# Performance work log

Hardware: AMD Instinct MI355X
Metric: run time of the kernel (lower is better)

Reference implementation:

```python
import jax, jax.numpy as jnp
import numpy as np
from jax import lax


def setup_inputs() -> dict:
    key = jax.random.key(0)
    ks = jax.random.split(key, 6)
    B, C, H, W = 8, 128, 64, 64   # C = 2*channel, channel (per-branch) c = 64
    c = C // 2
    return {
        "x_up": jax.random.normal(ks[0], (B, C, H, W), dtype=jnp.float32),
        "x_skip": jax.random.normal(ks[1], (B, C, H, W), dtype=jnp.float32),
        # nn.Linear(c, 2c): weight [out,in], bias [out]
        "kv1_w": jax.random.normal(ks[2], (2 * c, c), dtype=jnp.float32) * 0.05,
        "kv1_b": jnp.zeros((2 * c,), dtype=jnp.float32),
        "kv2_w": jax.random.normal(ks[3], (2 * c, c), dtype=jnp.float32) * 0.05,
        "kv2_b": jnp.zeros((2 * c,), dtype=jnp.float32),
        # Conv2d(2c, 2c, 3, stride 1, pad 1, bias=False), OIHW
        "conv_w": jax.random.normal(ks[4], (C, C, 3, 3), dtype=jnp.float32) * 0.05,
        # BatchNorm2d(2c) in inference form (running stats)
        "bn_gamma": jax.random.normal(ks[5], (C,), dtype=jnp.float32) * 0.1 + 1.0,
        "bn_beta": jnp.zeros((C,), dtype=jnp.float32),
        "bn_mean": jnp.zeros((C,), dtype=jnp.float32),
        "bn_var": jnp.ones((C,), dtype=jnp.float32),
    }


def reference(x_up, x_skip, kv1_w, kv1_b, kv2_w, kv2_b, conv_w,
              bn_gamma, bn_beta, bn_mean, bn_var):
    b, C, h, w = x_up.shape
    c = C // 2
    hw = h * w
    up1, up2 = x_up[:, :c], x_up[:, c:]
    sk1, sk2 = x_skip[:, :c], x_skip[:, c:]

    # ---- spatial attention branch (softmax over last axis, hw x hw) ----
    shortcut1 = up1 + sk1
    u1 = up1.reshape(b, c, hw).transpose(0, 2, 1)   # (b, hw, c)
    s1 = sk1.reshape(b, c, hw).transpose(0, 2, 1)   # (b, hw, c)
    kv = s1 @ kv1_w.T + kv1_b                        # (b, hw, 2c)
    k1, v1 = kv[..., :c], kv[..., c:]
    attn = jax.nn.softmax(jnp.einsum('bnc,bmc->bnm', u1, k1), axis=-1)  # (b, hw, hw)
    sout = jnp.einsum('bnm,bmc->bnc', attn, v1)      # (b, hw, c)
    sout = sout.transpose(0, 2, 1).reshape(b, c, h, w) + shortcut1

    # ---- channel attention branch (softmax over dim=1 of the c x c map) ----
    shortcut2 = up2 + sk2
    u2 = up2.reshape(b, c, hw).transpose(0, 2, 1)    # (b, hw, c)
    s2 = sk2.reshape(b, c, hw).transpose(0, 2, 1)
    kv = s2 @ kv2_w.T + kv2_b                        # (b, hw, 2c)
    k2, v2 = kv[..., :c], kv[..., c:]
    A = jax.nn.softmax(jnp.einsum('bnc,bnd->bcd', u2, k2), axis=1)  # (b, c, c)
    cout = jnp.einsum('bnc,bcd->bnd', v2, A)          # (b, hw, c)
    cout = cout.transpose(0, 2, 1).reshape(b, c, h, w) + shortcut2

    # ---- conv + BN (inference) + ReLU ----
    x = jnp.concatenate([sout, cout], axis=1)         # (b, 2c, h, w)
    y = lax.conv_general_dilated(x, conv_w, (1, 1), 'SAME',
                                 dimension_numbers=('NCHW', 'OIHW', 'NCHW'))
    inv = jax.lax.rsqrt(bn_var + 1e-5)
    y = (y - bn_mean[None, :, None, None]) * (inv * bn_gamma)[None, :, None, None] \
        + bn_beta[None, :, None, None]
    return jax.nn.relu(y)
```

## Files before the change

### kernel.cpp

```cpp
#include <hip/hip_runtime.h>
#include <math.h>

#define HW 4096

typedef __attribute__((ext_vector_type(8))) short bh8;
typedef __attribute__((ext_vector_type(4))) float f32x4;
typedef __attribute__((ext_vector_type(2))) unsigned int u32x2;
typedef unsigned int u32;
typedef unsigned short u16;

__device__ __forceinline__ u16 f2bf(float f) {
  union { float f; u32 u; } v; v.f = f;
  u32 u = v.u;
  return (u16)((u + 0x7FFFu + ((u >> 16) & 1u)) >> 16);
}
__device__ __forceinline__ float bf2f(u16 h) {
  union { u32 u; float f; } v; v.u = ((u32)h) << 16;
  return v.f;
}
__device__ __forceinline__ float ubits2f(u32 u) {
  union { u32 u; float f; } v; v.u = u;
  return v.f;
}
__device__ __forceinline__ u32 cvt_pk_bf16(float lo, float hi) {
  u32 r;
  asm("v_cvt_pk_bf16_f32 %0, %1, %2" : "=v"(r) : "v"(lo), "v"(hi));
  return r;
}
__device__ __forceinline__ float fexp2(float x) {
  float r;
  asm("v_exp_f32 %0, %1" : "=v"(r) : "v"(x));
  return r;
}

__global__ __launch_bounds__(256) void kv_proj(
    const float* __restrict__ xs,
    const float* __restrict__ w1, const float* __restrict__ b1,
    const float* __restrict__ w2, const float* __restrict__ b2,
    u32* __restrict__ Knm, u16* __restrict__ Vcm,
    u16* __restrict__ K2t, u16* __restrict__ V2t,
    const float* __restrict__ cw, const float* __restrict__ gamma,
    const float* __restrict__ beta, const float* __restrict__ mean,
    const float* __restrict__ var, u16* __restrict__ Wg,
    float* __restrict__ shb, float* __restrict__ M) {
  __shared__ __align__(16) u16 XsH[64][72];
  __shared__ __align__(16) u16 XsL[64][72];
  __shared__ u32 LtK[64][33];
  const int b = blockIdx.y, n0 = blockIdx.x * 64;
  const int t = threadIdx.x;
  const int wq = t >> 6, lane = t & 63, lq = lane & 15, quad = lane >> 4;
  const float* xsb = xs + (size_t)b * 128 * HW;

  {
    int gid = (blockIdx.y * 64 + blockIdx.x) * 256 + t;
    for (int i = gid; i < 147456; i += 131072) {
      int tap = i >> 14, oc = (i >> 7) & 127, ic = i & 127;
      float sc = gamma[oc] * rsqrtf(var[oc] + 1e-5f);
      Wg[i] = f2bf(cw[((size_t)(oc * 128 + ic)) * 9 + tap] * sc);
    }
    if (gid < 128) {
      float sc = gamma[gid] * rsqrtf(var[gid] + 1e-5f);
      shb[gid] = beta[gid] - mean[gid] * sc;
    }
    if (gid < 32768) M[gid] = 0.f;
  }

  for (int br = 0; br < 2; ++br) {
    const float* W = br ? w2 : w1;
    const float* bias = br ? b2 : b1;
    const float* src = xsb + (br ? 64 * HW : 0);

    bh8 wh[2][2], wl[2][2];
#pragma unroll
    for (int jt = 0; jt < 2; ++jt)
#pragma unroll
      for (int s = 0; s < 2; ++s) {
        const float* wr = W + (size_t)(wq * 32 + jt * 16 + lq) * 64 + s * 32 + quad * 8;
        float4 a0 = *(const float4*)wr;
        float4 a1 = *(const float4*)(wr + 4);
        float f[8] = {a0.x, a0.y, a0.z, a0.w, a1.x, a1.y, a1.z, a1.w};
        union { u32 u[4]; bh8 v; } H, L;
#pragma unroll
        for (int p = 0; p < 4; ++p) {
          u32 hp = cvt_pk_bf16(f[2 * p], f[2 * p + 1]);
          float h0 = ubits2f(hp << 16);
          float h1 = ubits2f(hp & 0xFFFF0000u);
          H.u[p] = hp;
          L.u[p] = cvt_pk_bf16(f[2 * p] - h0, f[2 * p + 1] - h1);
        }
        wh[jt][s] = H.v;
        wl[jt][s] = L.v;
      }

    if (br) __syncthreads();
    {
      const int n = t & 63, cg = t >> 6;
#pragma unroll
      for (int s8 = 0; s8 < 8; ++s8) {
        int ch0 = s8 * 8 + cg * 2;
        float f0 = src[(size_t)ch0 * HW + n0 + n];
        float f1 = src[(size_t)(ch0 + 1) * HW + n0 + n];
        u32 hp = cvt_pk_bf16(f0, f1);
        float h0 = ubits2f(hp << 16);
        float h1 = ubits2f(hp & 0xFFFF0000u);
        u32 lp = cvt_pk_bf16(f0 - h0, f1 - h1);
        *(u32*)&XsH[n][ch0] = hp;
        *(u32*)&XsL[n][ch0] = lp;
      }
    }
    __syncthreads();

    f32x4 acc[2][4];
#pragma unroll
    for (int nt = 0; nt < 4; ++nt) {
      const int xr = nt * 16 + lq;
      bh8 xh0 = *(const bh8*)&XsH[xr][quad * 8];
      bh8 xh1 = *(const bh8*)&XsH[xr][32 + quad * 8];
      bh8 xl0 = *(const bh8*)&XsL[xr][quad * 8];
      bh8 xl1 = *(const bh8*)&XsL[xr][32 + quad * 8];
#pragma unroll
      for (int jt = 0; jt < 2; ++jt) {
        f32x4 a = (f32x4)(0.f);
        a = __builtin_amdgcn_mfma_f32_16x16x32_bf16(wh[jt][0], xh0, a, 0, 0, 0);
        a = __builtin_amdgcn_mfma_f32_16x16x32_bf16(wh[jt][1], xh1, a, 0, 0, 0);
        a = __builtin_amdgcn_mfma_f32_16x16x32_bf16(wh[jt][0], xl0, a, 0, 0, 0);
        a = __builtin_amdgcn_mfma_f32_16x16x32_bf16(wh[jt][1], xl1, a, 0, 0, 0);
        a = __builtin_amdgcn_mfma_f32_16x16x32_bf16(wl[jt][0], xh0, a, 0, 0, 0);
        a = __builtin_amdgcn_mfma_f32_16x16x32_bf16(wl[jt][1], xh1, a, 0, 0, 0);
        acc[jt][nt] = a;
      }
    }

    if (br == 0) {
      if (wq < 2) {
#pragma unroll
        for (int jt = 0; jt < 2; ++jt) {
          float4 bv = *(const float4*)&bias[wq * 32 + jt * 16 + quad * 4];
#pragma unroll
          for (int nt = 0; nt < 4; ++nt) {
            f32x4 a = acc[jt][nt];
            LtK[nt * 16 + lq][wq * 16 + jt * 8 + quad * 2] =
                cvt_pk_bf16(a[0] + bv.x, a[1] + bv.y);
            LtK[nt * 16 + lq][wq * 16 + jt * 8 + quad * 2 + 1] =
                cvt_pk_bf16(a[2] + bv.z, a[3] + bv.w);
          }
        }
      } else {
#pragma unroll
        for (int jt = 0; jt < 2; ++jt) {
          float4 bv = *(const float4*)&bias[wq * 32 + jt * 16 + quad * 4];
          float bvv[4] = {bv.x, bv.y, bv.z, bv.w};
#pragma unroll
          for (int nt = 0; nt < 4; ++nt)
#pragma unroll
            for (int r = 0; r < 4; ++r) {
              int ch = (wq - 2) * 32 + jt * 16 + quad * 4 + r;
              Vcm[((size_t)b * 64 + ch) * HW + n0 + nt * 16 + lq] =
                  f2bf(acc[jt][nt][r] + bvv[r]);
            }
        }
      }
      __syncthreads();
#pragma unroll
      for (int p = 0; p < 8; ++p) {
        int idx = p * 256 + t;
        int n = idx >> 5, cc = idx & 31;
        Knm[((size_t)b * HW + n0 + n) * 32 + cc] = LtK[n][cc];
      }
    } else {
      u16* base = (wq < 2) ? (K2t + (size_t)b * 64 * HW) : (V2t + (size_t)b * 64 * HW);
      const int chb = (wq & 1) * 32;
#pragma unroll
      for (int jt = 0; jt < 2; ++jt) {
        float4 bv = *(const float4*)&bias[wq * 32 + jt * 16 + quad * 4];
        float bvv[4] = {bv.x, bv.y, bv.z, bv.w};
#pragma unroll
        for (int nt = 0; nt < 4; ++nt)
#pragma unroll
          for (int r = 0; r < 4; ++r) {
            int ch = chb + jt * 16 + quad * 4 + r;
            base[(size_t)ch * HW + n0 + nt * 16 + lq] =
                f2bf(acc[jt][nt][r] + bvv[r]);
          }
      }
    }
  }
}

__device__ __forceinline__ void qk_step(
    const bh8* kf, const bh8 (&qb)[4][2], f32x4 (&S)[2][4]) {
  __builtin_amdgcn_s_setprio(1);
#pragma unroll
  for (int mt = 0; mt < 2; ++mt)
#pragma unroll
    for (int nt = 0; nt < 4; ++nt) {
      f32x4 a = (f32x4)(0.f);
      a = __builtin_amdgcn_mfma_f32_16x16x32_bf16(kf[mt * 2 + 0], qb[nt][0], a, 0, 0, 0);
      a = __builtin_amdgcn_mfma_f32_16x16x32_bf16(kf[mt * 2 + 1], qb[nt][1], a, 0, 0, 0);
      S[mt][nt] = a;
    }
  __builtin_amdgcn_s_setprio(0);
}

__device__ __forceinline__ void sm_pv(
    const f32x4 (&S)[2][4], const bh8* vf, const bh8 ones,
    f32x4 (&O)[4][4], f32x4 (&Osum)[4]) {
#pragma unroll
  for (int nt = 0; nt < 4; ++nt) {
    const float c = 17.312340f;
    float e00 = fexp2(S[0][nt][0] - c), e01 = fexp2(S[0][nt][1] - c);
    float e02 = fexp2(S[0][nt][2] - c), e03 = fexp2(S[0][nt][3] - c);
    float e10 = fexp2(S[1][nt][0] - c), e11 = fexp2(S[1][nt][1] - c);
    float e12 = fexp2(S[1][nt][2] - c), e13 = fexp2(S[1][nt][3] - c);
    u32 A = cvt_pk_bf16(e00, e01);
    u32 B = cvt_pk_bf16(e02, e03);
    u32 C = cvt_pk_bf16(e10, e11);
    u32 D = cvt_pk_bf16(e12, e13);
    u32x2 rac = __builtin_amdgcn_permlane32_swap(A, C, 0, 0);
    u32x2 rbd = __builtin_amdgcn_permlane32_swap(B, D, 0, 0);
    u32x2 r02 = __builtin_amdgcn_permlane16_swap(rac.x, rac.y, 0, 0);
    u32x2 r13 = __builtin_amdgcn_permlane16_swap(rbd.x, rbd.y, 0, 0);
    union { u32 u[4]; bh8 v; } pb;
    pb.u[0] = r02.x;
    pb.u[1] = r13.x;
    pb.u[2] = r02.y;
    pb.u[3] = r13.y;
    __builtin_amdgcn_s_setprio(1);
#pragma unroll
    for (int ct = 0; ct < 4; ++ct)
      O[ct][nt] = __builtin_amdgcn_mfma_f32_16x16x32_bf16(vf[ct], pb.v, O[ct][nt], 0, 0, 0);
    Osum[nt] = __builtin_amdgcn_mfma_f32_16x16x32_bf16(ones, pb.v, Osum[nt], 0, 0, 0);
    __builtin_amdgcn_s_setprio(0);
  }
}

#define LOADKV(KB, KF, VF)                                            \
  do {                                                                \
    const int n0_ = (KB) * 128;                                       \
    const u16* kr_ = Kb + (size_t)(n0_ + wb + lq) * 64 + quad * 8;    \
    KF[0] = *(const bh8*)(kr_);                                       \
    KF[1] = *(const bh8*)(kr_ + 32);                                  \
    KF[2] = *(const bh8*)(kr_ + 1024);                                \
    KF[3] = *(const bh8*)(kr_ + 1056);                                \
    const u16* vr_ = Vb + (size_t)lq * HW + n0_ + wb + quad * 8;      \
    VF[0] = *(const bh8*)(vr_);                                       \
    VF[1] = *(const bh8*)(vr_ + 16 * HW);                             \
    VF[2] = *(const bh8*)(vr_ + 32 * HW);                             \
    VF[3] = *(const bh8*)(vr_ + 48 * HW);                             \
  } while (0)

__global__ __launch_bounds__(256, 2) void attn_gram(
    const float* __restrict__ xu, const float* __restrict__ xs,
    const u16* __restrict__ Knm, const u16* __restrict__ Vcm,
    u16* __restrict__ xcat,
    const u16* __restrict__ K2t, float* __restrict__ M) {
  __shared__ __align__(16) u16 SMEM[18432];
  const int b = blockIdx.y;
  const int t = threadIdx.x;
  const int wq = t >> 6, lane = t & 63, lq = lane & 15, quad = lane >> 4;

  if (blockIdx.x >= 64) {
    const int chunk = blockIdx.x - 64;
    const int nn = chunk * 128;
    const float* ub = xu + ((size_t)b * 128 + 64) * HW;
    const u16* kb2 = K2t + (size_t)b * 64 * HW;
    f32x4 acc[4];
#pragma unroll
    for (int ct = 0; ct < 4; ++ct) acc[ct] = (f32x4)(0.f);
#pragma unroll
    for (int kc = 0; kc < 4; ++kc) {
      const int nb2 = nn + kc * 32 + quad * 8;
      bh8 kb_ = *(const bh8*)&kb2[(size_t)(wq * 16 + lq) * HW + nb2];
#pragma unroll
      for (int ct = 0; ct < 4; ++ct) {
        const float* ar = ub + (size_t)(ct * 16 + lq) * HW + nb2;
        float4 a0 = *(const float4*)ar;
        float4 a1 = *(const float4*)(ar + 4);
        float f[8] = {a0.x, a0.y, a0.z, a0.w, a1.x, a1.y, a1.z, a1.w};
        union { u32 u[4]; bh8 v; } H, L;
#pragma unroll
        for (int p = 0; p < 4; ++p) {
          u32 hp = cvt_pk_bf16(f[2 * p], f[2 * p + 1]);
          float h0 = ubits2f(hp << 16);
          float h1 = ubits2f(hp & 0xFFFF0000u);
          H.u[p] = hp;
          L.u[p] = cvt_pk_bf16(f[2 * p] - h0, f[2 * p + 1] - h1);
        }
        acc[ct] = __builtin_amdgcn_mfma_f32_16x16x32_bf16(H.v, kb_, acc[ct], 0, 0, 0);
        acc[ct] = __builtin_amdgcn_mfma_f32_16x16x32_bf16(L.v, kb_, acc[ct], 0, 0, 0);
      }
    }
    float* Mb = M + (size_t)b * 4096;
#pragma unroll
    for (int ct = 0; ct < 4; ++ct)
#pragma unroll
      for (int r = 0; r < 4; ++r)
        atomicAdd(&Mb[(ct * 16 + quad * 4 + r) * 64 + wq * 16 + lq], acc[ct][r]);
    return;
  }

  const int q0 = blockIdx.x * 64;
  const int wb = wq * 32;
  const float* xub = xu + (size_t)b * 128 * HW;
  const float* xsb = xs + (size_t)b * 128 * HW;
  const u16* Kb = Knm + (size_t)b * HW * 64;
  const u16* Vb = Vcm + (size_t)b * 64 * HW;

  bh8 qb[4][2];
#pragma unroll
  for (int nt = 0; nt < 4; ++nt)
#pragma unroll
    for (int s = 0; s < 2; ++s)
#pragma unroll
      for (int j = 0; j < 8; ++j) {
        int ch = s * 32 + quad * 8 + j;
        qb[nt][s][j] =
            (short)f2bf(xub[(size_t)ch * HW + q0 + nt * 16 + lq] * 1.44269504f);
      }
  bh8 ones;
#pragma unroll
  for (int j = 0; j < 8; ++j) ones[j] = (short)0x3F80;

  f32x4 O[4][4];
#pragma unroll
  for (int ct = 0; ct < 4; ++ct)
#pragma unroll
    for (int nt = 0; nt < 4; ++nt) O[ct][nt] = (f32x4)(0.f);
  f32x4 Osum[4];
#pragma unroll
  for (int nt = 0; nt < 4; ++nt) Osum[nt] = (f32x4)(0.f);

  bh8 kfa[4], vfa[4], kfb[4], vfb[4];
  f32x4 Sa[2][4], Sb[2][4];
  LOADKV(0, kfa, vfa);
  qk_step(kfa, qb, Sa);
  LOADKV(1, kfb, vfb);
  for (int kb = 0; kb < 32; kb += 2) {
    qk_step(kfb, qb, Sb);
    sm_pv(Sa, vfa, ones, O, Osum);
    if (kb + 2 < 32) {
      LOADKV(kb + 2, kfa, vfa);
      qk_step(kfa, qb, Sa);
    }
    sm_pv(Sb, vfb, ones, O, Osum);
    if (kb + 3 < 32) LOADKV(kb + 3, kfb, vfb);
  }

  float* Posc = (float*)SMEM;
  float* Lred = (float*)(SMEM + 17408);
  if (quad == 0) {
#pragma unroll
    for (int nt = 0; nt < 4; ++nt) Lred[(wq * 4 + nt) * 16 + lq] = Osum[nt][0];
  }

  const int q = t & 63, cg = t >> 6;
#pragma unroll
  for (int rh = 0; rh < 2; ++rh) {
    if (rh) __syncthreads();
#pragma unroll
    for (int c2 = 0; c2 < 2; ++c2)
#pragma unroll
      for (int nt = 0; nt < 4; ++nt)
#pragma unroll
        for (int r = 0; r < 4; ++r)
          Posc[(wq * 32 + c2 * 16 + quad * 4 + r) * 68 + nt * 16 + lq] =
              O[rh * 2 + c2][nt][r];
    __syncthreads();
    float li = 0.f;
#pragma unroll
    for (int w2 = 0; w2 < 4; ++w2) li += Lred[w2 * 64 + q];
    float inv = 1.f / li;
    u16 h[8];
#pragma unroll
    for (int i = 0; i < 8; ++i) {
      int chl = cg * 8 + i;
      float s = 0.f;
#pragma unroll
      for (int w2 = 0; w2 < 4; ++w2) s += Posc[(w2 * 32 + chl) * 68 + q];
      int ch = rh * 32 + chl;
      size_t g = (size_t)ch * HW + q0 + q;
      h[i] = f2bf(s * inv + xub[g] + xsb[g]);
    }
    u32 pk[4];
#pragma unroll
    for (int j = 0; j < 4; ++j) pk[j] = (u32)h[2 * j] | ((u32)h[2 * j + 1] << 16);
    u16* ob = xcat + ((size_t)b * HW + q0 + q) * 128 + rh * 32 + cg * 8;
    *(uint4*)ob = make_uint4(pk[0], pk[1], pk[2], pk[3]);
  }
}

__global__ __launch_bounds__(256) void chan_apply(
    const u16* __restrict__ V2t, const float* __restrict__ M,
    const float* __restrict__ xu, const float* __restrict__ xs,
    u16* __restrict__ xcat) {
  __shared__ float Vsm[64][65];
  __shared__ float As[64][65];
  __shared__ float red1[4][64], red2[4][64];
  const int b = blockIdx.y, n0 = blockIdx.x * 64, t = threadIdx.x;
  const int lane = t & 63, dg = t >> 6;
  const u16* Vb = V2t + (size_t)b * 64 * HW;
  for (int s = 0; s < 16; ++s) {
    int c = s * 4 + dg;
    Vsm[lane][c] = bf2f(Vb[(size_t)c * HW + n0 + lane]);
  }
  for (int idx = t; idx < 4096; idx += 256) As[idx >> 6][idx & 63] = M[b * 4096 + idx];
  __syncthreads();
  float mx = -1e30f;
#pragma unroll
  for (int i = 0; i < 16; ++i) mx = fmaxf(mx, As[dg * 16 + i][lane]);
  red1[dg][lane] = mx;
  __syncthreads();
  mx = fmaxf(fmaxf(red1[0][lane], red1[1][lane]), fmaxf(red1[2][lane], red1[3][lane]));
  float se = 0.f;
#pragma unroll
  for (int i = 0; i < 16; ++i) {
    float e = __expf(As[dg * 16 + i][lane] - mx);
    As[dg * 16 + i][lane] = e;
    se += e;
  }
  red2[dg][lane] = se;
  __syncthreads();

  float acc[16];
#pragma unroll
  for (int i = 0; i < 16; ++i) acc[i] = 0.f;
  for (int c = 0; c < 64; ++c) {
    float v = Vsm[lane][c];
#pragma unroll
    for (int i = 0; i < 16; ++i) acc[i] = fmaf(v, As[c][dg * 16 + i], acc[i]);
  }
  const float* xub = xu + ((size_t)b * 128 + 64) * HW;
  const float* xsb = xs + ((size_t)b * 128 + 64) * HW;
  const int n = n0 + lane;
  u16 hv[16];
#pragma unroll
  for (int i = 0; i < 16; ++i) {
    int d = dg * 16 + i;
    float sm = red2[0][d] + red2[1][d] + red2[2][d] + red2[3][d];
    hv[i] = f2bf(acc[i] / sm + xub[(size_t)d * HW + n] + xsb[(size_t)d * HW + n]);
  }
  u32 pk[8];
#pragma unroll
  for (int j = 0; j < 8; ++j) pk[j] = (u32)hv[2 * j] | ((u32)hv[2 * j + 1] << 16);
  u16* ob = xcat + ((size_t)b * HW + n) * 128 + 64 + dg * 16;
  *(uint4*)(ob) = make_uint4(pk[0], pk[1], pk[2], pk[3]);
  *(uint4*)(ob + 8) = make_uint4(pk[4], pk[5], pk[6], pk[7]);
}

__global__ __launch_bounds__(512) void conv_mfma(
    const u16* __restrict__ X, const u16* __restrict__ Wg,
    const float* __restrict__ shb, float* __restrict__ out) {
  __shared__ __align__(16) u16 In[4 * 66 * 136];
  __shared__ __align__(16) u16 Wt[2][128 * 136];
  const int b = blockIdx.y, h0 = blockIdx.x * 2;
  const int t = threadIdx.x;
  const int wq = t >> 6, lane = t & 63, lq = lane & 15, quad = lane >> 4;
  const int nb = (wq & 1) * 64;
  const int mb = (wq >> 1) * 2;
  const u16* Xb = X + (size_t)b * HW * 128;

  if (t < 128) {
    int ih = t >> 5, iwsel = (t >> 4) & 1, ck = t & 15;
    int iw = iwsel ? 65 : 0;
    *(uint4*)&In[(ih * 66 + iw) * 136 + ck * 8] = make_uint4(0, 0, 0, 0);
  }
  for (int ih = 0; ih < 4; ++ih) {
    int h = h0 - 1 + ih;
    bool ok = (h >= 0 && h < 64);
    const u16* src = Xb + (size_t)h * 64 * 128;
#pragma unroll
    for (int p = 0; p < 2; ++p) {
      int idx = p * 512 + t;
      int row = idx >> 4, ck = idx & 15;
      uint4 d = make_uint4(0, 0, 0, 0);
      if (ok) d = *(const uint4*)(src + (size_t)row * 128 + ck * 8);
      *(uint4*)&In[(ih * 66 + 1 + row) * 136 + ck * 8] = d;
    }
  }
  {
    const u16* src = Wg;
#pragma unroll
    for (int p = 0; p < 4; ++p) {
      int idx = p * 512 + t;
      int oc = idx >> 4, ck = idx & 15;
      uint4 d = *(const uint4*)(src + oc * 128 + ck * 8);
      *(uint4*)&Wt[0][oc * 136 + ck * 8] = d;
    }
  }
  __syncthreads();

  f32x4 acc[2][4];
#pragma unroll
  for (int mt = 0; mt < 2; ++mt)
#pragma unroll
    for (int nt = 0; nt < 4; ++nt) acc[mt][nt] = (f32x4)(0.f);

  for (int tap = 0; tap < 9; ++tap) {
    const int cur = tap & 1;
    if (tap < 8) {
      const u16* src = Wg + (size_t)(tap + 1) * 128 * 128;
#pragma unroll
      for (int p = 0; p < 4; ++p) {
        int idx = p * 512 + t;
        int oc = idx >> 4, ck = idx & 15;
        uint4 d = *(const uint4*)(src + oc * 128 + ck * 8);
        *(uint4*)&Wt[cur ^ 1][oc * 136 + ck * 8] = d;
      }
    }
    const int dh = tap / 3, dw = tap - 3 * dh;
    const u16* Wc = &Wt[cur][0];
#pragma unroll
    for (int c = 0; c < 4; ++c) {
      bh8 bf[4];
#pragma unroll
      for (int nt = 0; nt < 4; ++nt)
        bf[nt] = *(const bh8*)&Wc[(nb + nt * 16 + lq) * 136 + c * 32 + quad * 8];
#pragma unroll
      for (int mt = 0; mt < 2; ++mt) {
        int s = (mb + mt) * 16 + lq;
        int ih = (s >> 6) + dh, iw = (s & 63) + dw;
        bh8 af = *(const bh8*)&In[(ih * 66 + iw) * 136 + c * 32 + quad * 8];
#pragma unroll
        for (int nt = 0; nt < 4; ++nt)
          acc[mt][nt] = __builtin_amdgcn_mfma_f32_16x16x32_bf16(af, bf[nt], acc[mt][nt], 0, 0, 0);
      }
    }
    __syncthreads();
  }

  float shv[4];
#pragma unroll
  for (int nt = 0; nt < 4; ++nt) shv[nt] = shb[nb + nt * 16 + lq];
#pragma unroll
  for (int mt = 0; mt < 2; ++mt) {
    int mtile = mb + mt;
    int h = h0 + (mtile >> 2);
    int w0 = ((mtile & 3) * 16) + quad * 4;
#pragma unroll
    for (int nt = 0; nt < 4; ++nt) {
      int oc = nb + nt * 16 + lq;
      float4 v;
      v.x = fmaxf(acc[mt][nt][0] + shv[nt], 0.f);
      v.y = fmaxf(acc[mt][nt][1] + shv[nt], 0.f);
      v.z = fmaxf(acc[mt][nt][2] + shv[nt], 0.f);
      v.w = fmaxf(acc[mt][nt][3] + shv[nt], 0.f);
      *(float4*)&out[((size_t)b * 128 + oc) * HW + h * 64 + w0] = v;
    }
  }
}

extern "C" void kernel_launch(void* const* d_in, const int* in_sizes, int n_in,
                              void* d_out, int out_size, void* d_ws, size_t ws_size,
                              hipStream_t stream) {
  const float* x_up   = (const float*)d_in[0];
  const float* x_skip = (const float*)d_in[1];
  const float* kv1_w  = (const float*)d_in[2];
  const float* kv1_b  = (const float*)d_in[3];
  const float* kv2_w  = (const float*)d_in[4];
  const float* kv2_b  = (const float*)d_in[5];
  const float* conv_w = (const float*)d_in[6];
  const float* bn_g   = (const float*)d_in[7];
  const float* bn_b   = (const float*)d_in[8];
  const float* bn_m   = (const float*)d_in[9];
  const float* bn_v   = (const float*)d_in[10];
  float* out = (float*)d_out;

  char* ws = (char*)d_ws;
  const size_t XCATB_B = (size_t)8 * HW * 128 * 2;
  const size_t KV16_B  = (size_t)8 * 64 * HW * 2;
  size_t off = 0;
  u16*   xcat = (u16*)(ws + off);   off += XCATB_B;
  u16*   K2t  = (u16*)(ws + off);   off += KV16_B;
  u16*   V2t  = (u16*)(ws + off);   off += KV16_B;
  u32*   Knm  = (u32*)(ws + off);   off += KV16_B;
  u16*   Vcm  = (u16*)(ws + off);   off += KV16_B;
  float* M    = (float*)(ws + off); off += (size_t)8 * 4096 * 4;
  u16*   Wg   = (u16*)(ws + off);   off += (size_t)9 * 128 * 128 * 2;
  float* shb  = (float*)(ws + off); off += 512;

  kv_proj<<<dim3(64, 8), 256, 0, stream>>>(x_skip, kv1_w, kv1_b, kv2_w, kv2_b,
                                           Knm, Vcm, K2t, V2t,
                                           conv_w, bn_g, bn_b, bn_m, bn_v, Wg,
                                           shb, M);
  attn_gram<<<dim3(96, 8), 256, 0, stream>>>(x_up, x_skip, (const u16*)Knm, Vcm,
                                             xcat, K2t, M);
  chan_apply<<<dim3(64, 8), 256, 0, stream>>>(V2t, M, x_up, x_skip, xcat);
  conv_mfma<<<dim3(32, 8), 512, 0, stream>>>(xcat, Wg, shb, out);
}
```

Measured before the change: 215.8 us.

## Flatten grids with batch-interleaved block ids and simplify attention pipeline

All four kernels now launch on a 1-D grid and derive the batch index from the low bits of the block id, so neighbouring blocks belong to different batches. On a multi-XCD GPU this spreads each batch's blocks across chiplets differently and changes L2 locality. The attention main loop also drops the software pipeline that overlapped QK of one tile with softmax/PV of the previous one. It replaces it with a fused per-tile step plus K/V prefetch, which lowers register pressure but gives up some MFMA/exp overlap.

Measured after the change: 207.1 us (median of 2 runs). 4.0% less time.

```diff
diff --git a/kernel.cpp b/kernel.cpp
--- a/kernel.cpp
+++ b/kernel.cpp
@@ -46,13 +46,14 @@
   __shared__ __align__(16) u16 XsH[64][72];
   __shared__ __align__(16) u16 XsL[64][72];
   __shared__ u32 LtK[64][33];
-  const int b = blockIdx.y, n0 = blockIdx.x * 64;
+  const int bid = blockIdx.x;
+  const int b = bid & 7, n0 = (bid >> 3) * 64;
   const int t = threadIdx.x;
   const int wq = t >> 6, lane = t & 63, lq = lane & 15, quad = lane >> 4;
   const float* xsb = xs + (size_t)b * 128 * HW;
 
   {
-    int gid = (blockIdx.y * 64 + blockIdx.x) * 256 + t;
+    int gid = bid * 256 + t;
     for (int i = gid; i < 147456; i += 131072) {
       int tap = i >> 14, oc = (i >> 7) & 127, ic = i & 127;
       float sc = gamma[oc] * rsqrtf(var[oc] + 1e-5f);
@@ -187,8 +188,10 @@
   }
 }
 
-__device__ __forceinline__ void qk_step(
-    const bh8* kf, const bh8 (&qb)[4][2], f32x4 (&S)[2][4]) {
+__device__ __forceinline__ void attn_step(
+    const bh8* kf, const bh8* vf, const bh8 (&qb)[4][2], const bh8 ones,
+    f32x4 (&O)[4][4], f32x4 (&Osum)[4]) {
+  f32x4 S[2][4];
   __builtin_amdgcn_s_setprio(1);
 #pragma unroll
   for (int mt = 0; mt < 2; ++mt)
@@ -200,11 +203,6 @@
       S[mt][nt] = a;
     }
   __builtin_amdgcn_s_setprio(0);
-}
-
-__device__ __forceinline__ void sm_pv(
-    const f32x4 (&S)[2][4], const bh8* vf, const bh8 ones,
-    f32x4 (&O)[4][4], f32x4 (&Osum)[4]) {
 #pragma unroll
   for (int nt = 0; nt < 4; ++nt) {
     const float c = 17.312340f;
@@ -255,12 +253,14 @@
     u16* __restrict__ xcat,
     const u16* __restrict__ K2t, float* __restrict__ M) {
   __shared__ __align__(16) u16 SMEM[18432];
-  const int b = blockIdx.y;
+  const int bid = blockIdx.x;
+  const int b = bid & 7;
+  const int x = bid >> 3;
   const int t = threadIdx.x;
   const int wq = t >> 6, lane = t & 63, lq = lane & 15, quad = lane >> 4;
 
-  if (blockIdx.x >= 64) {
-    const int chunk = blockIdx.x - 64;
+  if (x >= 64) {
+    const int chunk = x - 64;
     const int nn = chunk * 128;
     const float* ub = xu + ((size_t)b * 128 + 64) * HW;
     const u16* kb2 = K2t + (size_t)b * 64 * HW;
@@ -299,7 +299,7 @@
     return;
   }
 
-  const int q0 = blockIdx.x * 64;
+  const int q0 = x * 64;
   const int wb = wq * 32;
   const float* xub = xu + (size_t)b * 128 * HW;
   const float* xsb = xs + (size_t)b * 128 * HW;
@@ -331,19 +331,12 @@
   for (int nt = 0; nt < 4; ++nt) Osum[nt] = (f32x4)(0.f);
 
   bh8 kfa[4], vfa[4], kfb[4], vfb[4];
-  f32x4 Sa[2][4], Sb[2][4];
   LOADKV(0, kfa, vfa);
-  qk_step(kfa, qb, Sa);
-  LOADKV(1, kfb, vfb);
   for (int kb = 0; kb < 32; kb += 2) {
-    qk_step(kfb, qb, Sb);
-    sm_pv(Sa, vfa, ones, O, Osum);
-    if (kb + 2 < 32) {
-      LOADKV(kb + 2, kfa, vfa);
-      qk_step(kfa, qb, Sa);
-    }
-    sm_pv(Sb, vfb, ones, O, Osum);
-    if (kb + 3 < 32) LOADKV(kb + 3, kfb, vfb);
+    LOADKV(kb + 1, kfb, vfb);
+    attn_step(kfa, vfa, qb, ones, O, Osum);
+    if (kb + 2 < 32) LOADKV(kb + 2, kfa, vfa);
+    attn_step(kfb, vfb, qb, ones, O, Osum);
   }
 
   float* Posc = (float*)SMEM;
@@ -396,7 +389,8 @@
   __shared__ float Vsm[64][65];
   __shared__ float As[64][65];
   __shared__ float red1[4][64], red2[4][64];
-  const int b = blockIdx.y, n0 = blockIdx.x * 64, t = threadIdx.x;
+  const int bid = blockIdx.x;
+  const int b = bid & 7, n0 = (bid >> 3) * 64, t = threadIdx.x;
   const int lane = t & 63, dg = t >> 6;
   const u16* Vb = V2t + (size_t)b * 64 * HW;
   for (int s = 0; s < 16; ++s) {
@@ -452,7 +446,8 @@
     const float* __restrict__ shb, float* __restrict__ out) {
   __shared__ __align__(16) u16 In[4 * 66 * 136];
   __shared__ __align__(16) u16 Wt[2][128 * 136];
-  const int b = blockIdx.y, h0 = blockIdx.x * 2;
+  const int bid = blockIdx.x;
+  const int b = bid & 7, h0 = (bid >> 3) * 2;
   const int t = threadIdx.x;
   const int wq = t >> 6, lane = t & 63, lq = lane & 15, quad = lane >> 4;
   const int nb = (wq & 1) * 64;
@@ -578,12 +573,12 @@
   u16*   Wg   = (u16*)(ws + off);   off += (size_t)9 * 128 * 128 * 2;
   float* shb  = (float*)(ws + off); off += 512;
 
-  kv_proj<<<dim3(64, 8), 256, 0, stream>>>(x_skip, kv1_w, kv1_b, kv2_w, kv2_b,
-                                           Knm, Vcm, K2t, V2t,
-                                           conv_w, bn_g, bn_b, bn_m, bn_v, Wg,
-                                           shb, M);
-  attn_gram<<<dim3(96, 8), 256, 0, stream>>>(x_up, x_skip, (const u16*)Knm, Vcm,
-                                             xcat, K2t, M);
-  chan_apply<<<dim3(64, 8), 256, 0, stream>>>(V2t, M, x_up, x_skip, xcat);
-  conv_mfma<<<dim3(32, 8), 512, 0, stream>>>(xcat, Wg, shb, out);
-}
+  kv_proj<<<512, 256, 0, stream>>>(x_skip, kv1_w, kv1_b, kv2_w, kv2_b,
+                                   Knm, Vcm, K2t, V2t,
+                                   conv_w, bn_g, bn_b, bn_m, bn_v, Wg,
+                                   shb, M);
+  attn_gram<<<768, 256, 0, stream>>>(x_up, x_skip, (const u16*)Knm, Vcm,
+                                     xcat, K2t, M);
+  chan_apply<<<512, 256, 0, stream>>>(V2t, M, x_up, x_skip, xcat);
+  conv_mfma<<<256, 512, 0, stream>>>(xcat, Wg, shb, out);
+}
```
